# Optimization experiments

Hardware: AMD Instinct MI355X
Metric: run time of the kernel (lower is better)

## Reference

```python
import jax, jax.numpy as jnp
import numpy as np
from jax import lax

B, T = 16, 128
H, FD = 24, 4          # H hours, FD fourier harmonics
L = 64                 # latent_dim
D = 256                # d_model
NH = 8                 # heads
C = 1 + H * FD         # cont_dim = 97
EPS = 1e-5


def setup_inputs() -> dict:
    key = jax.random.key(0)
    ks = jax.random.split(key, 32)
    r = lambda k, sh, s: (jax.random.normal(k, sh, dtype=jnp.float32) * s)
    z = lambda sh: jnp.zeros(sh, dtype=jnp.float32)
    o = lambda sh: jnp.ones(sh, dtype=jnp.float32)
    return {
        'x_cont': jax.random.normal(ks[0], (B, T, C), dtype=jnp.float32),
        'z0': z((1, 1, L)),                       # learned initial hidden state
        'W_ih': r(ks[1], (L, 1), 0.1),            # RNN input weights
        'W_hh': r(ks[2], (L, L), 0.1),            # RNN recurrent weights
        'b_ih': z((L,)),
        'b_hh': z((L,)),
        'Uf': r(ks[3], (H, FD), 0.01),            # fourier coefficients
        'Wfp': r(ks[4], (L, H), 0.05),            # fourier_proj (L != H)
        'bfp': z((L,)),
        'feat_embed': r(ks[5], (L, D), 0.02),
        'W_in': r(ks[6], (3 * D, D), 0.02),       # MHA in_proj
        'b_in': z((3 * D,)),
        'W_ao': r(ks[7], (D, D), 0.02),           # MHA out_proj
        'b_ao': z((D,)),
        'g1': o((D,)), 'be1': z((D,)),            # ln1
        'W1': r(ks[8], (4 * D, D), 0.02), 'b1': z((4 * D,)),
        'W2': r(ks[9], (D, 4 * D), 0.02), 'b2': z((D,)),
        'g2': o((D,)), 'be2': z((D,)),            # ln2
        'Wop': r(ks[10], (1, D), 0.02), 'bop': z((1,)),   # out_proj d_model->1
        'Wg': r(ks[11], (L, L), 0.05), 'bg': z((L,)),     # gate
        'A': r(ks[12], (H, L), 0.01),
        'c': z((H,)),
    }


def _ln(x, g, b):
    mu = jnp.mean(x, -1, keepdims=True)
    var = jnp.mean(jnp.square(x - mu), -1, keepdims=True)
    return (x - mu) * lax.rsqrt(var + EPS) * g + b


def reference(x_cont, z0, W_ih, W_hh, b_ih, b_hh, Uf, Wfp, bfp, feat_embed,
              W_in, b_in, W_ao, b_ao, g1, be1, W1, b1, W2, b2, g2, be2,
              Wop, bop, Wg, bg, A, c):
    Bb, Tt, Cc = x_cont.shape
    x0 = x_cont[:, :, :1]              # (B,T,1)
    xf = x_cont[:, :, 1:]              # (B,T,H*FD)

    # --- single-layer relu RNN over time ---
    h0 = jnp.broadcast_to(z0[0, 0], (Bb, L))

    def step(h, x_t):                  # x_t: (B,1)
        h = jax.nn.relu(x_t @ W_ih.T + b_ih + h @ W_hh.T + b_hh)
        return h, h

    _, hs = lax.scan(step, h0, jnp.swapaxes(x0, 0, 1))
    h = jnp.swapaxes(hs, 0, 1)         # (B,T,L)

    # --- fourier features ---
    xf_mat = xf.reshape(Bb, Tt, H, FD)
    fourier_h = jnp.einsum('bthf,hf->bth', xf_mat, Uf)   # (B,T,H)
    z = h + fourier_h @ Wfp.T + bfp                      # (B,T,L)

    # --- feature attention: tokens (B*T, L, D) ---
    N = Bb * Tt
    zf = z.reshape(N, L)
    tokens = zf[:, :, None] * feat_embed[None]           # (N,L,D)

    qkv = tokens @ W_in.T + b_in                         # (N,L,3D)
    q, k, v = jnp.split(qkv, 3, axis=-1)
    dh = D // NH
    split_heads = lambda t: t.reshape(N, L, NH, dh).transpose(0, 2, 1, 3)
    q, k, v = split_heads(q), split_heads(k), split_heads(v)
    att = jax.nn.softmax(jnp.einsum('nhqd,nhkd->nhqk', q, k) / np.sqrt(dh), axis=-1)
    ao = jnp.einsum('nhqk,nhkd->nhqd', att, v).transpose(0, 2, 1, 3).reshape(N, L, D)
    ao = ao @ W_ao.T + b_ao

    t1 = _ln(tokens + ao, g1, be1)
    ffn = jax.nn.relu(t1 @ W1.T + b1) @ W2.T + b2
    t2 = _ln(t1 + ffn, g2, be2)
    delta = (t2 @ Wop.T + bop)[..., 0].reshape(Bb, Tt, L)

    gate = jax.nn.sigmoid(z @ Wg.T + bg)
    z_out = z + gate * delta

    o = z_out @ A.T + c                                  # (B,T,H)
    return (o, z_out)
```

## Files before the change

### kernel.cpp

```cpp
#include <hip/hip_runtime.h>

typedef short bf16x8 __attribute__((ext_vector_type(8)));
typedef float f32x4  __attribute__((ext_vector_type(4)));

__device__ __forceinline__ unsigned short f2b(float f){
  union { float f; unsigned u; } v; v.f = f;
  unsigned r = v.u + 0x7FFFu + ((v.u >> 16) & 1u);
  return (unsigned short)(r >> 16);
}
__device__ __forceinline__ float b2f(unsigned short s){
  union { unsigned u; float f; } v; v.u = ((unsigned)s) << 16;
  return v.f;
}
__device__ __forceinline__ unsigned pk2(float lo, float hi){
  unsigned r;
  asm("v_cvt_pk_bf16_f32 %0, %1, %2" : "=v"(r) : "v"(lo), "v"(hi));
  return r;
}

__global__ void k_pre_qkv(const float* __restrict__ FE, const float* __restrict__ W_in,
                          float* __restrict__ Qm, float* __restrict__ Km, float* __restrict__ Vm){
  int id = blockIdx.x*256 + threadIdx.x;
  int part = id >> 14;
  int l = (id >> 8) & 63;
  int d = id & 255;
  const float4* fe = (const float4*)(FE + l*256);
  const float4* wr = (const float4*)(W_in + (part*256 + d)*256);
  float s = 0.f;
  #pragma unroll 8
  for (int k=0;k<64;k++){
    float4 a = fe[k], b = wr[k];
    s += a.x*b.x + a.y*b.y + a.z*b.z + a.w*b.w;
  }
  float* dst = (part==0)?Qm:((part==1)?Km:Vm);
  dst[l*256+d] = s;
}

__global__ void k_pre2(const float* __restrict__ Qm, const float* __restrict__ Km,
                       const float* __restrict__ Vm,
                       const float* __restrict__ b_in, const float* __restrict__ W_ao,
                       const float* __restrict__ b_ao, const float* __restrict__ FE,
                       float* __restrict__ Gc, float* __restrict__ U,
                       float* __restrict__ W, float* __restrict__ S,
                       float* __restrict__ abias, short* __restrict__ M2c,
                       const float* __restrict__ W1, const float* __restrict__ W2,
                       short* __restrict__ W1c, short* __restrict__ W2c,
                       float* __restrict__ FEc,
                       const float* __restrict__ x_cont, const float* __restrict__ z0,
                       const float* __restrict__ W_ih, const float* __restrict__ W_hh,
                       const float* __restrict__ b_ih, const float* __restrict__ b_hh,
                       const float* __restrict__ Uf, const float* __restrict__ Wfp,
                       const float* __restrict__ bfp, float* __restrict__ zout){
  int bid = blockIdx.x;
  int tid = threadIdx.x;
  const float inv = 0.17677669529663687f * 1.4426950408889634f;
  if (bid < 16){
    int b = bid;
    int l = tid;
    bool act = (l < 64);
    __shared__ float h_sh[64];
    __shared__ float fh_sh[24];
    __shared__ float WfpT[24][64];
    float wr[64];
    float wih=0, bb=0, bf=0;
    float uf0=0,uf1=0,uf2=0,uf3=0;
    if (act){
      #pragma unroll
      for (int j=0;j<64;j++) wr[j] = W_hh[l*64+j];
      #pragma unroll
      for (int j=0;j<24;j++) WfpT[j][l] = Wfp[l*24+j];
      wih = W_ih[l];
      bb  = b_ih[l] + b_hh[l];
      bf  = bfp[l];
      if (l < 24){ uf0=Uf[l*4+0]; uf1=Uf[l*4+1]; uf2=Uf[l*4+2]; uf3=Uf[l*4+3]; }
      h_sh[l] = z0[l];
    }
    __syncthreads();
    const float* xb = x_cont + (size_t)b*128*97;
    for (int t=0;t<128;t++){
      float hn = 0.f, fh = 0.f;
      if (act){
        float x0 = xb[t*97];
        float a0=0,a1=0,a2=0,a3=0;
        #pragma unroll
        for (int j=0;j<64;j+=4){
          a0 += wr[j  ]*h_sh[j  ];
          a1 += wr[j+1]*h_sh[j+1];
          a2 += wr[j+2]*h_sh[j+2];
          a3 += wr[j+3]*h_sh[j+3];
        }
        hn = fmaxf(x0*wih + bb + ((a0+a1)+(a2+a3)), 0.f);
        if (l < 24){
          const float* xf = xb + t*97 + 1 + l*4;
          fh = xf[0]*uf0 + xf[1]*uf1 + xf[2]*uf2 + xf[3]*uf3;
        }
      }
      __syncthreads();
      if (act){
        h_sh[l] = hn;
        if (l < 24) fh_sh[l] = fh;
      }
      __syncthreads();
      if (act){
        float zv = hn + bf;
        #pragma unroll
        for (int j=0;j<24;j++) zv += fh_sh[j]*WfpT[j][l];
        zout[((size_t)b*128 + t)*64 + l] = zv;
      }
    }
    return;
  }
  if (bid < 214){
    int id = (bid-16)*256 + tid;
    if (id < 32768){
      int h = id >> 12, ks = (id>>11)&1, w4 = (id>>9)&3, lane = (id>>3)&63, j = id&7;
      int lq = w4*16 + (lane&15);
      int lk = ks*32 + (lane>>4)*8 + j;
      const float* qp = Qm + lq*256 + h*32;
      const float* kp = Km + lk*256 + h*32;
      float s=0.f;
      #pragma unroll
      for (int d=0;d<32;d++) s += qp[d]*kp[d];
      Gc[id] = s*inv;
    } else if (id < 33280){
      int j = id - 32768; int h = j>>6, lq = j&63;
      const float* qp = Qm + lq*256 + h*32;
      const float* bk = b_in + 256 + h*32;
      float s=0.f;
      #pragma unroll
      for (int d=0;d<32;d++) s += qp[d]*bk[d];
      U[j] = s*inv;
    } else if (id < 33792){
      int j = id - 33280; int h = j>>6, lk = j&63;
      const float* kp = Km + lk*256 + h*32;
      const float* bq = b_in + h*32;
      float s=0.f;
      #pragma unroll
      for (int d=0;d<32;d++) s += bq[d]*kp[d];
      W[j] = s*inv;
    } else if (id < 33800){
      int h = id - 33792;
      float s=0.f;
      #pragma unroll
      for (int d=0;d<32;d++) s += b_in[h*32+d]*b_in[256+h*32+d];
      S[h] = s*inv;
    } else if (id < 34056){
      int e = id - 33800;
      float s = b_ao[e];
      for (int d=0; d<256; d++) s += b_in[512+d]*W_ao[e*256+d];
      abias[e] = s;
    } else if (id < 50440){
      int o = id - 34056;
      int tt = o>>12, et = (o>>10)&3, w4 = (o>>8)&3, lane = (o>>2)&63, j = o&3;
      int row = tt*16 + (lane&15);
      int col = w4*64 + et*16 + (lane>>4)*4 + j;
      FEc[o] = FE[row*256 + col];
    }
    return;
  }
  if (bid < 726){
    int o = (bid-214)*256 + tid;
    int h = o>>14, ks = (o>>13)&1, w4 = (o>>11)&3, et = (o>>9)&3, lane = (o>>3)&63, j = o&7;
    int e = w4*64 + et*16 + (lane&15);
    int lk = ks*32 + (lane>>4)*8 + j;
    const float* vp = Vm + lk*256 + h*32;
    const float* wp = W_ao + e*256 + h*32;
    float s=0.f;
    #pragma unroll
    for (int d=0;d<32;d++) s += vp[d]*wp[d];
    M2c[o] = (short)f2b(s);
    return;
  }
  {
    int id3 = (bid-726)*256 + tid;
    if (id3 < 262144){
      int row = id3 >> 8, col = id3 & 255;
      int c = row >> 7, w4 = (row>>5)&3, ct = (row>>4)&1, lrow = row & 15;
      int ks = col >> 5, lhi = (col>>3)&3, j = col & 7;
      int o = c*32768 + ks*4096 + w4*1024 + ct*512 + (lhi*16+lrow)*8 + j;
      W1c[o] = (short)f2b(W1[id3]);
    } else {
      int idx = id3 - 262144;
      int row = idx >> 10, col = idx & 1023;
      int w4 = row >> 6, et = (row>>4)&3, lrow = row & 15;
      int c = col >> 7, ks2 = (col>>5)&3, lhi = (col>>3)&3, j = col & 7;
      int o = c*32768 + ks2*8192 + w4*2048 + et*512 + (lhi*16+lrow)*8 + j;
      W2c[o] = (short)f2b(W2[idx]);
    }
    return;
  }
}

__global__ __launch_bounds__(256, 3) void k_main(
  const float* __restrict__ zall, const float* __restrict__ Gc,
  const float* __restrict__ Ubuf, const float* __restrict__ Wbuf, const float* __restrict__ Sbuf,
  const float* __restrict__ abias, const short* __restrict__ M2c,
  const float* __restrict__ FEc,
  const short* __restrict__ W1c, const float* __restrict__ b1,
  const short* __restrict__ W2c, const float* __restrict__ b2,
  const float* __restrict__ g1, const float* __restrict__ be1,
  const float* __restrict__ g2, const float* __restrict__ be2,
  const float* __restrict__ Wop, const float* __restrict__ bop,
  const float* __restrict__ Wg, const float* __restrict__ bg,
  const float* __restrict__ Amat, const float* __restrict__ cvec,
  float* __restrict__ out)
{
  const int n = blockIdx.x;
  const int tid = threadIdx.x;
  const int w = tid >> 6, lane = tid & 63, lg = lane >> 4, lr = lane & 15;
  const int cb = w * 64;

  __shared__ __align__(16) short t1_sh[64][264];
  __shared__ __align__(16) char  upool[17408];
  __shared__ float redA[4][64];
  __shared__ float redB[4][64];
  __shared__ float gate_sh[64];
  __shared__ float z_sh[64];

  short (*mid_sh)[136] = reinterpret_cast<short (*)[136]>(upool);
  short (*pa_sh)[4][2][64][8] = reinterpret_cast<short (*)[4][2][64][8]>(upool);

  if (tid < 64) z_sh[tid] = zall[n*64 + tid];
  __syncthreads();

  float zkf[16];
  #pragma unroll
  for (int i=0;i<16;i++) zkf[i] = z_sh[(i>>3)*32 + lg*8 + (i&7)];

  {
    const int glq = tid >> 2, gq = tid & 3;
    float p = 0.f;
    const f32x4* wg = (const f32x4*)(Wg + glq*64 + gq*16);
    const f32x4* zv4 = (const f32x4*)(z_sh + gq*16);
    #pragma unroll
    for (int i=0;i<4;i++){
      f32x4 wv = wg[i], zv = zv4[i];
      p += wv[0]*zv[0] + wv[1]*zv[1] + wv[2]*zv[2] + wv[3]*zv[3];
    }
    p += __shfl_xor(p, 1);
    p += __shfl_xor(p, 2);
    if (gq == 0) gate_sh[glq] = 1.f/(1.f + __expf(-(p + bg[glq])));
  }

  f32x4 acc[4][4];
  #pragma unroll
  for (int et=0;et<4;et++)
    #pragma unroll
    for (int tt=0;tt<4;tt++){ f32x4 zz = {0.f,0.f,0.f,0.f}; acc[et][tt] = zz; }

  const int lq_own = w*16 + lr;
  const float zq_own = z_sh[lq_own];
  float zqzk[16];
  #pragma unroll
  for (int i=0;i<16;i++) zqzk[i] = zq_own * zkf[i];

  #pragma unroll 1
  for (int h=0; h<8; ++h){
    {
      const float base = zq_own * Ubuf[h*64 + lq_own] + Sbuf[h];
      float e0[16];
      #pragma unroll
      for (int ks=0;ks<2;ks++){
        const float* gbase = Gc + h*4096 + ks*2048 + w*512 + lane*8;
        f32x4 ga = *(const f32x4*)(gbase);
        f32x4 gb = *(const f32x4*)(gbase + 4);
        f32x4 wa = *(const f32x4*)(Wbuf + h*64 + ks*32 + lg*8);
        f32x4 wb = *(const f32x4*)(Wbuf + h*64 + ks*32 + lg*8 + 4);
        #pragma unroll
        for (int j=0;j<4;j++){
          e0[ks*8+j]   = exp2f(fmaf(zqzk[ks*8+j],   ga[j], fmaf(zkf[ks*8+j],   wa[j], base)));
          e0[ks*8+4+j] = exp2f(fmaf(zqzk[ks*8+4+j], gb[j], fmaf(zkf[ks*8+4+j], wb[j], base)));
        }
      }
      float sum = 0.f;
      #pragma unroll
      for (int i=0;i<16;i++) sum += e0[i];
      sum += __shfl_xor(sum,16);
      sum += __shfl_xor(sum,32);
      float inv = __builtin_amdgcn_rcpf(sum);
      #pragma unroll
      for (int ks=0;ks<2;ks++){
        union { bf16x8 v; unsigned u[4]; } pa;
        #pragma unroll
        for (int p=0;p<4;p++)
          pa.u[p] = pk2(e0[ks*8+2*p]*inv*zkf[ks*8+2*p], e0[ks*8+2*p+1]*inv*zkf[ks*8+2*p+1]);
        *(bf16x8*)&pa_sh[h&1][w][ks][lane][0] = pa.v;
      }
    }
    __syncthreads();
    __builtin_amdgcn_s_setprio(1);
    #pragma unroll
    for (int ks=0; ks<2; ks++){
      bf16x8 am[4], bt[4];
      #pragma unroll
      for (int et=0;et<4;et++)
        am[et] = *(const bf16x8*)(M2c + h*16384 + ks*8192 + w*2048 + et*512 + lane*8);
      #pragma unroll
      for (int tt=0;tt<4;tt++) bt[tt] = *(const bf16x8*)&pa_sh[h&1][tt][ks][lane][0];
      #pragma unroll
      for (int et=0;et<4;et++)
        #pragma unroll
        for (int tt=0;tt<4;tt++)
          acc[et][tt] = __builtin_amdgcn_mfma_f32_16x16x32_bf16(am[et], bt[tt], acc[et][tt], 0,0,0);
    }
    __builtin_amdgcn_s_setprio(0);
  }

  f32x4 ab4[4], g14[4], be14[4];
  #pragma unroll
  for (int et=0;et<4;et++){
    int e0_ = cb + et*16 + lg*4;
    ab4[et]  = *(const f32x4*)(abias + e0_);
    g14[et]  = *(const f32x4*)(g1 + e0_);
    be14[et] = *(const f32x4*)(be1 + e0_);
  }
  float sum1[4], ssq1[4];
  #pragma unroll
  for (int tt=0;tt<4;tt++){
    int tok = tt*16 + lr;
    float zt = z_sh[tok];
    float s = 0.f, sq = 0.f;
    #pragma unroll
    for (int et=0;et<4;et++){
      f32x4 fe = *(const f32x4*)(FEc + tt*4096 + et*1024 + w*256 + lane*4);
      #pragma unroll
      for (int r=0;r<4;r++){
        float v = acc[et][tt][r] + ab4[et][r] + zt*fe[r];
        acc[et][tt][r] = v; s += v; sq += v*v;
      }
    }
    s  += __shfl_xor(s,16);  s  += __shfl_xor(s,32);
    sq += __shfl_xor(sq,16); sq += __shfl_xor(sq,32);
    sum1[tt] = s; ssq1[tt] = sq;
  }
  if (lane < 16){
    #pragma unroll
    for (int tt=0;tt<4;tt++){ redA[w][tt*16+lane] = sum1[tt]; redB[w][tt*16+lane] = ssq1[tt]; }
  }
  __syncthreads();
  float mu1[4], rs1[4];
  #pragma unroll
  for (int tt=0;tt<4;tt++){
    int tok = tt*16 + lr;
    float s  = redA[0][tok] + redA[1][tok] + redA[2][tok] + redA[3][tok];
    float sq = redB[0][tok] + redB[1][tok] + redB[2][tok] + redB[3][tok];
    float m = s * (1.f/256.f);
    mu1[tt] = m;
    rs1[tt] = rsqrtf(sq*(1.f/256.f) - m*m + 1e-5f);
  }
  #pragma unroll
  for (int et=0;et<4;et++)
    #pragma unroll
    for (int tt=0;tt<4;tt++){
      uint2 p;
      float v0 = (acc[et][tt][0]-mu1[tt])*rs1[tt]*g14[et][0] + be14[et][0];
      float v1 = (acc[et][tt][1]-mu1[tt])*rs1[tt]*g14[et][1] + be14[et][1];
      float v2 = (acc[et][tt][2]-mu1[tt])*rs1[tt]*g14[et][2] + be14[et][2];
      float v3 = (acc[et][tt][3]-mu1[tt])*rs1[tt]*g14[et][3] + be14[et][3];
      p.x = pk2(v0,v1); p.y = pk2(v2,v3);
      *(uint2*)&t1_sh[tt*16+lr][cb + et*16 + lg*4] = p;
    }
  __syncthreads();

  #pragma unroll
  for (int et=0;et<4;et++)
    #pragma unroll
    for (int tt=0;tt<4;tt++){ f32x4 zz = {0.f,0.f,0.f,0.f}; acc[et][tt] = zz; }

  #pragma unroll 1
  for (int c=0; c<8; c++){
    f32x4 midv[2][4];
    #pragma unroll
    for (int ct=0;ct<2;ct++){
      f32x4 bi = *(const f32x4*)(b1 + c*128 + w*32 + ct*16 + lg*4);
      #pragma unroll
      for (int tt=0;tt<4;tt++) midv[ct][tt] = bi;
    }
    #pragma unroll
    for (int ks=0; ks<8; ks++){
      bf16x8 bt[4], aw[2];
      #pragma unroll
      for (int tt=0;tt<4;tt++) bt[tt] = *(const bf16x8*)&t1_sh[tt*16+lr][ks*32 + lg*8];
      #pragma unroll
      for (int ct=0;ct<2;ct++)
        aw[ct] = *(const bf16x8*)(W1c + c*32768 + ks*4096 + w*1024 + ct*512 + lane*8);
      #pragma unroll
      for (int ct=0;ct<2;ct++)
        #pragma unroll
        for (int tt=0;tt<4;tt++)
          midv[ct][tt] = __builtin_amdgcn_mfma_f32_16x16x32_bf16(aw[ct], bt[tt], midv[ct][tt], 0,0,0);
    }
    __syncthreads();
    #pragma unroll
    for (int ct=0;ct<2;ct++)
      #pragma unroll
      for (int tt=0;tt<4;tt++){
        uint2 p;
        p.x = pk2(fmaxf(midv[ct][tt][0],0.f), fmaxf(midv[ct][tt][1],0.f));
        p.y = pk2(fmaxf(midv[ct][tt][2],0.f), fmaxf(midv[ct][tt][3],0.f));
        *(uint2*)&mid_sh[tt*16+lr][w*32 + ct*16 + lg*4] = p;
      }
    __syncthreads();
    __builtin_amdgcn_s_setprio(1);
    #pragma unroll
    for (int ks2=0; ks2<4; ks2++){
      bf16x8 aw2[4], bm[4];
      #pragma unroll
      for (int et=0;et<4;et++)
        aw2[et] = *(const bf16x8*)(W2c + c*32768 + ks2*8192 + w*2048 + et*512 + lane*8);
      #pragma unroll
      for (int tt=0;tt<4;tt++) bm[tt] = *(const bf16x8*)&mid_sh[tt*16+lr][ks2*32 + lg*8];
      #pragma unroll
      for (int et=0;et<4;et++)
        #pragma unroll
        for (int tt=0;tt<4;tt++)
          acc[et][tt] = __builtin_amdgcn_mfma_f32_16x16x32_bf16(aw2[et], bm[tt], acc[et][tt], 0,0,0);
    }
    __builtin_amdgcn_s_setprio(0);
  }

  f32x4 b24[4], g24[4], be24[4], wop4[4];
  #pragma unroll
  for (int et=0;et<4;et++){
    int e0_ = cb + et*16 + lg*4;
    b24[et]  = *(const f32x4*)(b2 + e0_);
    g24[et]  = *(const f32x4*)(g2 + e0_);
    be24[et] = *(const f32x4*)(be2 + e0_);
    wop4[et] = *(const f32x4*)(Wop + e0_);
  }
  float sum2[4], ssq2[4];
  #pragma unroll
  for (int tt=0;tt<4;tt++){
    int tok = tt*16 + lr;
    float s = 0.f, sq = 0.f;
    #pragma unroll
    for (int et=0;et<4;et++){
      uint2 t1v = *(const uint2*)&t1_sh[tok][cb + et*16 + lg*4];
      #pragma unroll
      for (int r=0;r<4;r++){
        unsigned short hs = (unsigned short)((r&1) ? ((r<2?t1v.x:t1v.y)>>16) : ((r<2?t1v.x:t1v.y)&0xFFFF));
        float v = acc[et][tt][r] + b24[et][r] + b2f(hs);
        acc[et][tt][r] = v; s += v; sq += v*v;
      }
    }
    s  += __shfl_xor(s,16);  s  += __shfl_xor(s,32);
    sq += __shfl_xor(sq,16); sq += __shfl_xor(sq,32);
    sum2[tt] = s; ssq2[tt] = sq;
  }
  if (lane < 16){
    #pragma unroll
    for (int tt=0;tt<4;tt++){ redA[w][tt*16+lane] = sum2[tt]; redB[w][tt*16+lane] = ssq2[tt]; }
  }
  __syncthreads();

  float dpart[4];
  #pragma unroll
  for (int tt=0;tt<4;tt++){
    int tok = tt*16 + lr;
    float s  = redA[0][tok] + redA[1][tok] + redA[2][tok] + redA[3][tok];
    float sq = redB[0][tok] + redB[1][tok] + redB[2][tok] + redB[3][tok];
    float m = s * (1.f/256.f);
    float rs = rsqrtf(sq*(1.f/256.f) - m*m + 1e-5f);
    float d = 0.f;
    #pragma unroll
    for (int et=0;et<4;et++)
      #pragma unroll
      for (int r=0;r<4;r++){
        float t2 = (acc[et][tt][r]-m)*rs*g24[et][r] + be24[et][r];
        d += t2*wop4[et][r];
      }
    d += __shfl_xor(d,16); d += __shfl_xor(d,32);
    dpart[tt] = d;
  }
  __syncthreads();
  if (lane < 16){
    #pragma unroll
    for (int tt=0;tt<4;tt++) redA[w][tt*16+lane] = dpart[tt];
  }
  __syncthreads();
  if (tid < 64){
    float delta = redA[0][tid]+redA[1][tid]+redA[2][tid]+redA[3][tid] + bop[0];
    float zo = z_sh[tid] + gate_sh[tid]*delta;
    out[49152 + (size_t)n*64 + tid] = zo;
    z_sh[tid] = zo;
  }
  __syncthreads();
  if (tid < 24){
    const float* ar = Amat + tid*64;
    float s = cvec[tid];
    #pragma unroll
    for (int j=0;j<64;j++) s += z_sh[j]*ar[j];
    out[(size_t)n*24 + tid] = s;
  }
}

extern "C" void kernel_launch(void* const* d_in, const int* in_sizes, int n_in,
                              void* d_out, int out_size, void* d_ws, size_t ws_size,
                              hipStream_t stream) {
  const float* x_cont = (const float*)d_in[0];
  const float* z0    = (const float*)d_in[1];
  const float* W_ih  = (const float*)d_in[2];
  const float* W_hh  = (const float*)d_in[3];
  const float* b_ih  = (const float*)d_in[4];
  const float* b_hh  = (const float*)d_in[5];
  const float* Uf    = (const float*)d_in[6];
  const float* Wfp   = (const float*)d_in[7];
  const float* bfp   = (const float*)d_in[8];
  const float* FE    = (const float*)d_in[9];
  const float* W_in  = (const float*)d_in[10];
  const float* b_in  = (const float*)d_in[11];
  const float* W_ao  = (const float*)d_in[12];
  const float* b_ao  = (const float*)d_in[13];
  const float* g1    = (const float*)d_in[14];
  const float* be1   = (const float*)d_in[15];
  const float* W1    = (const float*)d_in[16];
  const float* b1    = (const float*)d_in[17];
  const float* W2    = (const float*)d_in[18];
  const float* b2    = (const float*)d_in[19];
  const float* g2    = (const float*)d_in[20];
  const float* be2   = (const float*)d_in[21];
  const float* Wop   = (const float*)d_in[22];
  const float* bop   = (const float*)d_in[23];
  const float* Wg    = (const float*)d_in[24];
  const float* bg    = (const float*)d_in[25];
  const float* Amat  = (const float*)d_in[26];
  const float* cvec  = (const float*)d_in[27];
  float* out = (float*)d_out;
  char* ws = (char*)d_ws;

  float* z    = (float*)(ws + 0);
  float* Qm   = (float*)(ws + 524288);
  float* Km   = (float*)(ws + 589824);
  float* Vm   = (float*)(ws + 655360);
  float* Gc   = (float*)(ws + 720896);
  float* U    = (float*)(ws + 851968);
  float* Wb   = (float*)(ws + 854016);
  float* S    = (float*)(ws + 856064);
  float* ab   = (float*)(ws + 856320);
  short* M2c  = (short*)(ws + 857344);
  short* W1c  = (short*)(ws + 1119488);
  short* W2c  = (short*)(ws + 1643776);
  float* FEc  = (float*)(ws + 2168064);

  hipLaunchKernelGGL(k_pre_qkv, dim3(192), dim3(256), 0, stream, FE, W_in, Qm, Km, Vm);
  hipLaunchKernelGGL(k_pre2, dim3(2774), dim3(256), 0, stream,
                     Qm, Km, Vm, b_in, W_ao, b_ao, FE, Gc, U, Wb, S, ab, M2c,
                     W1, W2, W1c, W2c, FEc,
                     x_cont, z0, W_ih, W_hh, b_ih, b_hh, Uf, Wfp, bfp, z);
  hipLaunchKernelGGL(k_main, dim3(2048), dim3(256), 0, stream, z, Gc, U, Wb, S, ab, M2c, FEc,
                     W1c, b1, W2c, b2, g1, be1, g2, be2, Wop, bop, Wg, bg, Amat, cvec, out);
}
```

Measured before the change: 317.6 us.

## Hoist non-recurrent RNN input and Fourier projection out of serial time loop

The input projection (x0*W_ih+biases) and the Fourier feature projection through Wfp are now computed in parallel by extra blocks of the first pre-kernel and written to workspace arrays. The serial 128-step RNN loop in k_pre2 only reads these precomputed values, which removes the 24-term dot product and the strided x_cont loads from each step. In exchange there is extra global traffic for two B*T*64 float arrays and more blocks in the first kernel.

```diff
diff --git a/kernel.cpp b/kernel.cpp
--- a/kernel.cpp
+++ b/kernel.cpp
@@ -18,22 +18,52 @@
   return r;
 }
 
-__global__ void k_pre_qkv(const float* __restrict__ FE, const float* __restrict__ W_in,
-                          float* __restrict__ Qm, float* __restrict__ Km, float* __restrict__ Vm){
-  int id = blockIdx.x*256 + threadIdx.x;
-  int part = id >> 14;
-  int l = (id >> 8) & 63;
-  int d = id & 255;
-  const float4* fe = (const float4*)(FE + l*256);
-  const float4* wr = (const float4*)(W_in + (part*256 + d)*256);
-  float s = 0.f;
-  #pragma unroll 8
-  for (int k=0;k<64;k++){
-    float4 a = fe[k], b = wr[k];
-    s += a.x*b.x + a.y*b.y + a.z*b.z + a.w*b.w;
-  }
-  float* dst = (part==0)?Qm:((part==1)?Km:Vm);
-  dst[l*256+d] = s;
+__global__ void k_pre1(const float* __restrict__ FE, const float* __restrict__ W_in,
+                       float* __restrict__ Qm, float* __restrict__ Km, float* __restrict__ Vm,
+                       const float* __restrict__ x_cont,
+                       const float* __restrict__ W_ih,
+                       const float* __restrict__ b_ih, const float* __restrict__ b_hh,
+                       const float* __restrict__ Uf, const float* __restrict__ Wfp,
+                       const float* __restrict__ bfp,
+                       float* __restrict__ preA, float* __restrict__ fzA){
+  int bid = blockIdx.x;
+  int tid = threadIdx.x;
+  if (bid < 192){
+    int id = bid*256 + tid;
+    int part = id >> 14;
+    int l = (id >> 8) & 63;
+    int d = id & 255;
+    const float4* fe = (const float4*)(FE + l*256);
+    const float4* wr = (const float4*)(W_in + (part*256 + d)*256);
+    float s = 0.f;
+    #pragma unroll 8
+    for (int k=0;k<64;k++){
+      float4 a = fe[k], b = wr[k];
+      s += a.x*b.x + a.y*b.y + a.z*b.z + a.w*b.w;
+    }
+    float* dst = (part==0)?Qm:((part==1)?Km:Vm);
+    dst[l*256+d] = s;
+    return;
+  }
+  {
+    int g = tid >> 6, l = tid & 63;
+    int n = (bid-192)*4 + g;
+    __shared__ float Wfp_sh[64][24];
+    __shared__ float fh_sh[4][24];
+    for (int i=tid; i<1536; i+=256) Wfp_sh[i/24][i%24] = Wfp[i];
+    const float* xr = x_cont + (size_t)n*97;
+    float x0 = xr[0];
+    if (l < 24){
+      float fh = xr[1+l*4]*Uf[l*4] + xr[2+l*4]*Uf[l*4+1] + xr[3+l*4]*Uf[l*4+2] + xr[4+l*4]*Uf[l*4+3];
+      fh_sh[g][l] = fh;
+    }
+    __syncthreads();
+    float s = bfp[l];
+    #pragma unroll
+    for (int j=0;j<24;j++) s += fh_sh[g][j]*Wfp_sh[l][j];
+    fzA[(size_t)n*64 + l] = s;
+    preA[(size_t)n*64 + l] = x0*W_ih[l] + b_ih[l] + b_hh[l];
+  }
 }
 
 __global__ void k_pre2(const float* __restrict__ Qm, const float* __restrict__ Km,
@@ -46,11 +76,9 @@
                        const float* __restrict__ W1, const float* __restrict__ W2,
                        short* __restrict__ W1c, short* __restrict__ W2c,
                        float* __restrict__ FEc,
-                       const float* __restrict__ x_cont, const float* __restrict__ z0,
-                       const float* __restrict__ W_ih, const float* __restrict__ W_hh,
-                       const float* __restrict__ b_ih, const float* __restrict__ b_hh,
-                       const float* __restrict__ Uf, const float* __restrict__ Wfp,
-                       const float* __restrict__ bfp, float* __restrict__ zout){
+                       const float* __restrict__ z0, const float* __restrict__ W_hh,
+                       const float* __restrict__ preA, const float* __restrict__ fzA,
+                       float* __restrict__ zout){
   int bid = blockIdx.x;
   int tid = threadIdx.x;
   const float inv = 0.17677669529663687f * 1.4426950408889634f;
@@ -59,28 +87,21 @@
     int l = tid;
     bool act = (l < 64);
     __shared__ float h_sh[64];
-    __shared__ float fh_sh[24];
-    __shared__ float WfpT[24][64];
     float wr[64];
-    float wih=0, bb=0, bf=0;
-    float uf0=0,uf1=0,uf2=0,uf3=0;
     if (act){
       #pragma unroll
       for (int j=0;j<64;j++) wr[j] = W_hh[l*64+j];
-      #pragma unroll
-      for (int j=0;j<24;j++) WfpT[j][l] = Wfp[l*24+j];
-      wih = W_ih[l];
-      bb  = b_ih[l] + b_hh[l];
-      bf  = bfp[l];
-      if (l < 24){ uf0=Uf[l*4+0]; uf1=Uf[l*4+1]; uf2=Uf[l*4+2]; uf3=Uf[l*4+3]; }
       h_sh[l] = z0[l];
     }
     __syncthreads();
-    const float* xb = x_cont + (size_t)b*128*97;
+    const float* pb = preA + (size_t)b*128*64;
+    const float* fb = fzA  + (size_t)b*128*64;
+    float* zb = zout + (size_t)b*128*64;
     for (int t=0;t<128;t++){
-      float hn = 0.f, fh = 0.f;
+      float hn = 0.f, fz = 0.f;
       if (act){
-        float x0 = xb[t*97];
+        float pre = pb[t*64 + l];
+        fz = fb[t*64 + l];
         float a0=0,a1=0,a2=0,a3=0;
         #pragma unroll
         for (int j=0;j<64;j+=4){
@@ -89,24 +110,14 @@
           a2 += wr[j+2]*h_sh[j+2];
           a3 += wr[j+3]*h_sh[j+3];
         }
-        hn = fmaxf(x0*wih + bb + ((a0+a1)+(a2+a3)), 0.f);
-        if (l < 24){
-          const float* xf = xb + t*97 + 1 + l*4;
-          fh = xf[0]*uf0 + xf[1]*uf1 + xf[2]*uf2 + xf[3]*uf3;
-        }
+        hn = fmaxf(pre + ((a0+a1)+(a2+a3)), 0.f);
       }
       __syncthreads();
       if (act){
         h_sh[l] = hn;
-        if (l < 24) fh_sh[l] = fh;
       }
       __syncthreads();
-      if (act){
-        float zv = hn + bf;
-        #pragma unroll
-        for (int j=0;j<24;j++) zv += fh_sh[j]*WfpT[j][l];
-        zout[((size_t)b*128 + t)*64 + l] = zv;
-      }
+      if (act) zb[t*64 + l] = hn + fz;
     }
     return;
   }
@@ -541,12 +552,16 @@
   short* W1c  = (short*)(ws + 1119488);
   short* W2c  = (short*)(ws + 1643776);
   float* FEc  = (float*)(ws + 2168064);
-
-  hipLaunchKernelGGL(k_pre_qkv, dim3(192), dim3(256), 0, stream, FE, W_in, Qm, Km, Vm);
+  float* preA = (float*)(ws + 2233600);
+  float* fzA  = (float*)(ws + 2757888);
+
+  hipLaunchKernelGGL(k_pre1, dim3(704), dim3(256), 0, stream,
+                     FE, W_in, Qm, Km, Vm,
+                     x_cont, W_ih, b_ih, b_hh, Uf, Wfp, bfp, preA, fzA);
   hipLaunchKernelGGL(k_pre2, dim3(2774), dim3(256), 0, stream,
                      Qm, Km, Vm, b_in, W_ao, b_ao, FE, Gc, U, Wb, S, ab, M2c,
                      W1, W2, W1c, W2c, FEc,
-                     x_cont, z0, W_ih, W_hh, b_ih, b_hh, Uf, Wfp, bfp, z);
+                     z0, W_hh, preA, fzA, z);
   hipLaunchKernelGGL(k_main, dim3(2048), dim3(256), 0, stream, z, Gc, U, Wb, S, ab, M2c, FEc,
                      W1c, b1, W2c, b2, g1, be1, g2, be2, Wop, bop, Wg, bg, Amat, cvec, out);
 }
```

After: 292.1 us. 8.0% less time.
